# Kernel tuning notes

Measured on AMD Instinct MI355X. Metric: run time of the kernel, lower is better.

Reference implementation:

```python
import jax, jax.numpy as jnp
import numpy as np

N_NODES = 100000
N_EDGES = 1600000


def gcn_conv(x, W, b, src, dst, ew, n):
    """PyG GCNConv: x@W, symmetric deg^-1/2 norm with self-loops, scatter-add at dst, +b."""
    loop = jnp.arange(n, dtype=src.dtype)
    s = jnp.concatenate([src, loop])            # sources incl. self-loops
    d = jnp.concatenate([dst, loop])            # targets incl. self-loops
    w = jnp.concatenate([ew, jnp.ones((n,), ew.dtype)])  # self-loop weight = 1
    deg = jax.ops.segment_sum(w, d, num_segments=n)      # weighted in-degree
    dinv = jnp.where(deg > 0, jax.lax.rsqrt(deg), 0.0)
    norm = dinv[s] * w * dinv[d]                # [E+N]
    h = x @ W                                   # [N, F_out]
    msg = h[s] * norm[:, None]                  # gather + per-edge scale
    out = jax.ops.segment_sum(msg, d, num_segments=n)    # scatter-add
    return out + b


def setup_inputs() -> dict:
    key = jax.random.key(0)
    ks = jax.random.split(key, 8)
    in_dim, hid, lat = 128, 128, 64
    x = jax.random.normal(ks[0], (N_NODES, in_dim), jnp.float32)
    edge_index = jax.random.randint(ks[1], (2, N_EDGES), 0, N_NODES, dtype=jnp.int32)
    weights = jax.random.uniform(ks[2], (N_EDGES,), jnp.float32)
    s_in = 1.0 / np.sqrt(in_dim)
    s_h = 1.0 / np.sqrt(hid)
    return {
        "x": x,
        "edge_index": edge_index,
        "weights": weights,
        "W1": jax.random.normal(ks[3], (in_dim, hid), jnp.float32) * s_in,
        "b1": jnp.zeros((hid,), jnp.float32),
        "W2": jax.random.normal(ks[4], (hid, hid), jnp.float32) * s_h,
        "b2": jnp.zeros((hid,), jnp.float32),
        "W_mu": jax.random.normal(ks[5], (hid, lat), jnp.float32) * s_h,
        "b_mu": jnp.zeros((lat,), jnp.float32),
        "W_lv": jax.random.normal(ks[6], (hid, lat), jnp.float32) * s_h,
        "b_lv": jnp.zeros((lat,), jnp.float32),
    }


def reference(x, edge_index, weights, W1, b1, W2, b2, W_mu, b_mu, W_lv, b_lv):
    n = x.shape[0]
    src, dst = edge_index[0], edge_index[1]
    h = jax.nn.relu(gcn_conv(x, W1, b1, src, dst, weights, n))
    h = gcn_conv(h, W2, b2, src, dst, weights, n)
    g = jnp.mean(h, axis=0, keepdims=True)      # [1, hid] global mean pool
    mu = g @ W_mu + b_mu
    logvar = g @ W_lv + b_lv
    return (mu, logvar)
```

## Files before the change

kernel.cpp:

```cpp
#include <hip/hip_runtime.h>


typedef __bf16 bf16x8 __attribute__((ext_vector_type(8)));
typedef float f32x4 __attribute__((ext_vector_type(4)));
typedef float f32x2 __attribute__((ext_vector_type(2)));
typedef unsigned long long u64;

#define RE   2048
#define BSH  8
#define BCAP 5120
#define NBMX 392

__device__ __forceinline__ float bf2f(unsigned short u){
  return __uint_as_float(((unsigned)u) << 16);
}
__device__ __forceinline__ unsigned short f2bf(float f){
  unsigned u = __float_as_uint(f);
  u += 0x7fffu + ((u >> 16) & 1u);
  return (unsigned short)(u >> 16);
}
__device__ __forceinline__ __bf16 us2bf(unsigned short u){
  __bf16 b; __builtin_memcpy(&b, &u, 2); return b;
}
__device__ __forceinline__ float ldf(const void* p, int i, int isf32){
  return isf32 ? ((const float*)p)[i] : bf2f(((const unsigned short*)p)[i]);
}
__device__ __forceinline__ void fma8f8(float* acc, float n, uint2 h){
  f32x2 p0 = __builtin_amdgcn_cvt_pk_f32_fp8((int)h.x, false);
  f32x2 p1 = __builtin_amdgcn_cvt_pk_f32_fp8((int)h.x, true);
  f32x2 p2 = __builtin_amdgcn_cvt_pk_f32_fp8((int)h.y, false);
  f32x2 p3 = __builtin_amdgcn_cvt_pk_f32_fp8((int)h.y, true);
  acc[0] = fmaf(n, p0[0], acc[0]);
  acc[1] = fmaf(n, p0[1], acc[1]);
  acc[2] = fmaf(n, p1[0], acc[2]);
  acc[3] = fmaf(n, p1[1], acc[3]);
  acc[4] = fmaf(n, p2[0], acc[4]);
  acc[5] = fmaf(n, p2[1], acc[5]);
  acc[6] = fmaf(n, p3[0], acc[6]);
  acc[7] = fmaf(n, p3[1], acc[7]);
}

__device__ __forceinline__ void scanBuckets(int* __restrict__ cnt, int* __restrict__ sm,
    int* __restrict__ hrow, int* __restrict__ rrow, int NB, int tid){
  const int K = (NBMX + 255) / 256;
  int c0 = tid * K;
  int loc = 0;
  #pragma unroll
  for (int i = 0; i < K; ++i){
    int j = c0 + i;
    if (j < NB) loc += cnt[j];
  }
  sm[tid] = loc;
  __syncthreads();
  for (int off = 1; off < 256; off <<= 1){
    int tmp = (tid >= off) ? sm[tid - off] : 0;
    __syncthreads();
    sm[tid] += tmp;
    __syncthreads();
  }
  int running = sm[tid] - loc;
  #pragma unroll
  for (int i = 0; i < K; ++i){
    int j = c0 + i;
    if (j < NB){
      int old = cnt[j];
      hrow[j] = old;
      rrow[j] = running;
      cnt[j] = running;
      running += old;
    }
  }
}

__global__ void k_init(const unsigned* __restrict__ xw, int* __restrict__ flag,
                       const void* __restrict__ W1, unsigned short* __restrict__ W1T,
                       float* __restrict__ v){
  __shared__ int s[256];
  int t = threadIdx.x;
  int cnt = 0;
  for (int k = t; k < 4096; k += 256){
    unsigned lo = xw[k] & 0xFFFFu;
    int e = (int)((lo >> 7) & 0xFFu);
    if ((e >= 100 && e <= 141) || (lo & 0x7FFFu) == 0) cnt++;
  }
  s[t] = cnt;
  __syncthreads();
  for (int off = 128; off > 0; off >>= 1){
    if (t < off) s[t] += s[t + off];
    __syncthreads();
  }
  int isf32 = (s[0] < 2458) ? 1 : 0;
  if (blockIdx.x == 0){
    if (t == 0) *flag = isf32;
    if (t < 128) v[t] = 0.0f;
  }
  int gid = blockIdx.x * 256 + t;
  int k = gid & 127, n = gid >> 7;
  W1T[gid] = isf32 ? f2bf(((const float*)W1)[k * 128 + n])
                   : ((const unsigned short*)W1)[k * 128 + n];
}

__global__ void __launch_bounds__(256) k_binG(const int* __restrict__ src,
    const int* __restrict__ dst, const void* __restrict__ w,
    u64* __restrict__ stagD, u64* __restrict__ stagS,
    int* __restrict__ histD, int* __restrict__ roffD,
    int* __restrict__ histS, int* __restrict__ roffS,
    int E, int NB, int NR,
    const void* __restrict__ xv, const __bf16* __restrict__ wt,
    unsigned char* __restrict__ H, int N, const int* __restrict__ flagp){
  __shared__ int cntD[NBMX];
  __shared__ int cntS[NBMX];
  __shared__ u64 stag[RE];
  __shared__ int sm[256];
  int tid = threadIdx.x;
  if ((int)blockIdx.x >= NR){
    int gb = (int)blockIdx.x - NR;
    int wave = (gb * 256 + tid) >> 6;
    int lane = tid & 63;
    int row16 = wave << 4;
    if (row16 >= N) return;
    int isf32 = *flagp;
    int m = lane & 15, q = lane >> 4;
    bf16x8 a0, a1, a2, a3;
    if (isf32){
      const float* ap = (const float*)xv + (size_t)(row16 + m) * 128 + q * 8;
      #pragma unroll
      for (int j = 0; j < 8; ++j){
        a0[j] = us2bf(f2bf(ap[j +  0]));
        a1[j] = us2bf(f2bf(ap[j + 32]));
        a2[j] = us2bf(f2bf(ap[j + 64]));
        a3[j] = us2bf(f2bf(ap[j + 96]));
      }
    } else {
      const __bf16* ap = (const __bf16*)xv + (size_t)(row16 + m) * 128 + q * 8;
      a0 = *(const bf16x8*)(ap +  0);
      a1 = *(const bf16x8*)(ap + 32);
      a2 = *(const bf16x8*)(ap + 64);
      a3 = *(const bf16x8*)(ap + 96);
    }
    for (int nt = 0; nt < 8; ++nt){
      const __bf16* bp = wt + (size_t)(nt * 16 + m) * 128 + q * 8;
      bf16x8 b0 = *(const bf16x8*)(bp +  0);
      bf16x8 b1 = *(const bf16x8*)(bp + 32);
      bf16x8 b2 = *(const bf16x8*)(bp + 64);
      bf16x8 b3 = *(const bf16x8*)(bp + 96);
      f32x4 acc = {0.f, 0.f, 0.f, 0.f};
      acc = __builtin_amdgcn_mfma_f32_16x16x32_bf16(a0, b0, acc, 0, 0, 0);
      acc = __builtin_amdgcn_mfma_f32_16x16x32_bf16(a1, b1, acc, 0, 0, 0);
      acc = __builtin_amdgcn_mfma_f32_16x16x32_bf16(a2, b2, acc, 0, 0, 0);
      acc = __builtin_amdgcn_mfma_f32_16x16x32_bf16(a3, b3, acc, 0, 0, 0);
      unsigned char* op = H + (size_t)(row16 + q * 4) * 128 + nt * 16 + m;
      op[0]   = (unsigned char)(__builtin_amdgcn_cvt_pk_fp8_f32(acc[0], acc[0], 0, false) & 0xFF);
      op[128] = (unsigned char)(__builtin_amdgcn_cvt_pk_fp8_f32(acc[1], acc[1], 0, false) & 0xFF);
      op[256] = (unsigned char)(__builtin_amdgcn_cvt_pk_fp8_f32(acc[2], acc[2], 0, false) & 0xFF);
      op[384] = (unsigned char)(__builtin_amdgcn_cvt_pk_fp8_f32(acc[3], acc[3], 0, false) & 0xFF);
    }
    return;
  }
  int r = blockIdx.x;
  for (int i = tid; i < NB; i += 256){ cntD[i] = 0; cntS[i] = 0; }
  __syncthreads();
  int isf32 = *flagp;
  int e0 = r * RE;
  int en = E - e0; if (en > RE) en = RE;
  u64 rec[8];
  #pragma unroll
  for (int k = 0; k < 8; ++k){
    int o = k * 256 + tid;
    rec[k] = ~0ull;
    if (o < en){
      int idx = e0 + o;
      int s_ = src[idx], d_ = dst[idx];
      float wf = ldf(w, idx, isf32);
      int wq = (int)(wf * 32768.0f + 0.5f);
      if (wq > 32767) wq = 32767;
      rec[k] = ((u64)(unsigned)d_ << 32) | ((u64)(unsigned)s_ << 15) | (unsigned)wq;
      atomicAdd(&cntD[d_ >> BSH], 1);
      atomicAdd(&cntS[s_ >> BSH], 1);
    }
  }
  __syncthreads();
  scanBuckets(cntD, sm, histD + (size_t)r * NB, roffD + (size_t)r * NB, NB, tid);
  __syncthreads();
  #pragma unroll
  for (int k = 0; k < 8; ++k){
    if (rec[k] != ~0ull){
      int p = atomicAdd(&cntD[(int)(rec[k] >> 32) >> BSH], 1);
      stag[p] = rec[k];
    }
  }
  __syncthreads();
  u64* opD = stagD + (size_t)r * RE;
  for (int i = tid; i < en; i += 256) opD[i] = stag[i];
  __syncthreads();
  scanBuckets(cntS, sm, histS + (size_t)r * NB, roffS + (size_t)r * NB, NB, tid);
  __syncthreads();
  #pragma unroll
  for (int k = 0; k < 8; ++k){
    if (rec[k] != ~0ull){
      int d_ = (int)(rec[k] >> 32);
      int s_ = (int)((rec[k] >> 15) & 0x1FFFFu);
      unsigned wq = (unsigned)(rec[k] & 32767u);
      u64 rs = ((u64)(unsigned)s_ << 32) | ((u64)(unsigned)d_ << 15) | wq;
      int p = atomicAdd(&cntS[s_ >> BSH], 1);
      stag[p] = rs;
    }
  }
  __syncthreads();
  u64* opS = stagS + (size_t)r * RE;
  for (int i = tid; i < en; i += 256) opS[i] = stag[i];
}

__global__ void __launch_bounds__(256) k_transp4(const int* __restrict__ A,
    const int* __restrict__ B, const int* __restrict__ C, const int* __restrict__ D,
    int* __restrict__ AT, int* __restrict__ BT, int* __restrict__ CT,
    int* __restrict__ DT, int NR, int NB){
  __shared__ int ta[32][33];
  __shared__ int tb[32][33];
  __shared__ int tc[32][33];
  __shared__ int td[32][33];
  int bx = (int)blockIdx.x * 32;
  int by = (int)blockIdx.y * 32;
  int tx = threadIdx.x & 31, ty = threadIdx.x >> 5;
  for (int yy = ty; yy < 32; yy += 8){
    int r = by + yy, b = bx + tx;
    int v1 = 0, v2 = 0, v3 = 0, v4 = 0;
    if (r < NR && b < NB){
      size_t o = (size_t)r * NB + b;
      v1 = A[o]; v2 = B[o]; v3 = C[o]; v4 = D[o];
    }
    ta[yy][tx] = v1; tb[yy][tx] = v2; tc[yy][tx] = v3; td[yy][tx] = v4;
  }
  __syncthreads();
  for (int yy = ty; yy < 32; yy += 8){
    int b = bx + yy, r = by + tx;
    if (b < NB && r < NR){
      size_t o = (size_t)b * NR + r;
      AT[o] = ta[tx][yy]; BT[o] = tb[tx][yy];
      CT[o] = tc[tx][yy]; DT[o] = td[tx][yy];
    }
  }
}

__global__ void __launch_bounds__(512) k_pass2a(const u64* __restrict__ staging,
    const int* __restrict__ histT, const int* __restrict__ roffT,
    float* __restrict__ dinv, int* __restrict__ cnt, int* __restrict__ rowptr,
    int* __restrict__ bsum, int NR, int N){
  __shared__ unsigned cd[256];
  __shared__ int sm[512];
  int b = blockIdx.x, tid = threadIdx.x;
  int lo = b << BSH;
  int nn = N - lo; if (nn > 256) nn = 256;
  if (tid < 256) cd[tid] = 0u;
  __syncthreads();
  const int* hrow = histT + (size_t)b * NR;
  const int* rrow = roffT + (size_t)b * NR;
  for (int r = tid; r < NR; r += 512){
    int len = hrow[r];
    if (len == 0) continue;
    const u64* rp = staging + (size_t)r * RE + rrow[r];
    for (int k = 0; k < len; ++k){
      u64 rec = rp[k];
      int dl = (int)(rec >> 32) - lo;
      atomicAdd(&cd[dl], (1u << 20) | (unsigned)((rec & 32767u) >> 2));
    }
  }
  __syncthreads();
  int val = 0;
  if (tid < nn){
    unsigned p = cd[tid];
    dinv[lo + tid] = rsqrtf(1.0f + (float)(p & 0xFFFFFu) * (1.0f / 8192.0f));
    cnt[lo + tid] = (int)(p >> 20);
    val = (int)(p >> 20);
  }
  sm[tid] = val;
  __syncthreads();
  for (int off = 1; off < 512; off <<= 1){
    int tmp = (tid >= off) ? sm[tid - off] : 0;
    __syncthreads();
    sm[tid] += tmp;
    __syncthreads();
  }
  if (tid < nn) rowptr[lo + tid] = sm[tid] - val;
  if (tid == 511) bsum[b] = sm[511];
}

__global__ void k_scanB(const int* __restrict__ bsum, int* __restrict__ boffs, int NB){
  __shared__ int s[512];
  int t = threadIdx.x;
  int val = (t < NB) ? bsum[t] : 0;
  s[t] = val;
  __syncthreads();
  for (int off = 1; off < 512; off <<= 1){
    int tmp = (t >= off) ? s[t - off] : 0;
    __syncthreads();
    s[t] += tmp;
    __syncthreads();
  }
  boffs[t] = s[t] - val;
}

__global__ void k_scanC(int* __restrict__ rowptr, const int* __restrict__ boffs,
                        unsigned* __restrict__ edges, int E, int N){
  if (blockIdx.x == 0 && threadIdx.x >= 240)
    edges[E + threadIdx.x - 240] = 0u;
  int i = blockIdx.x * 256 + threadIdx.x;
  if (i >= N) return;
  rowptr[i] = rowptr[i] + boffs[blockIdx.x];
}

__global__ void __launch_bounds__(512) k_post(const u64* __restrict__ stagD,
    const int* __restrict__ histDT, const int* __restrict__ roffDT,
    const u64* __restrict__ stagS, const int* __restrict__ histST,
    const int* __restrict__ roffST, const float* __restrict__ dinv,
    const int* __restrict__ rowptr, const int* __restrict__ cnt,
    unsigned* __restrict__ edges, float2* __restrict__ dc, int2* __restrict__ rc,
    int NR, int N){
  __shared__ unsigned recs[BCAP];
  __shared__ int cur[256];
  __shared__ int sb[2];
  int b = (int)blockIdx.x >> 1, tid = threadIdx.x;
  int lo = b << BSH;
  int nn = N - lo; if (nn > 256) nn = 256;
  if (blockIdx.x & 1){
    float* SL = (float*)recs;
    if (tid < 256) SL[tid] = 0.0f;
    __syncthreads();
    const int* hrow = histST + (size_t)b * NR;
    const int* rrow = roffST + (size_t)b * NR;
    for (int r = tid; r < NR; r += 512){
      int len = hrow[r];
      if (len == 0) continue;
      const u64* rp = stagS + (size_t)r * RE + rrow[r];
      for (int k = 0; k < len; ++k){
        u64 rec = rp[k];
        int s_ = (int)(rec >> 32);
        int d_ = (int)((rec >> 15) & 0x1FFFFu);
        float wqf = (float)(rec & 32767u) * (1.0f / 32768.0f);
        atomicAdd(&SL[s_ - lo], wqf * dinv[d_]);
      }
    }
    __syncthreads();
    if (tid < nn){
      int i = lo + tid;
      float di = dinv[i];
      dc[i] = make_float2(di * di, di * di + di * SL[tid]);
      rc[i] = make_int2(rowptr[i], cnt[i]);
    }
    return;
  }
  if (tid == 0){
    int base = rowptr[lo];
    sb[0] = base;
    sb[1] = rowptr[lo + nn - 1] + cnt[lo + nn - 1] - base;
  }
  __syncthreads();
  int base = sb[0], tot = sb[1];
  if (tot > BCAP) tot = BCAP;
  if (tid < nn) cur[tid] = rowptr[lo + tid] - base;
  __syncthreads();
  const int* hrow = histDT + (size_t)b * NR;
  const int* rrow = roffDT + (size_t)b * NR;
  for (int r = tid; r < NR; r += 512){
    int len = hrow[r];
    if (len == 0) continue;
    const u64* rp = stagD + (size_t)r * RE + rrow[r];
    for (int k = 0; k < len; ++k){
      u64 rec = rp[k];
      int d_ = (int)(rec >> 32);
      int s_ = (int)((rec >> 15) & 0x1FFFFu);
      int wq = (int)(rec & 32767u);
      float nrm = dinv[s_] * ((float)wq * (1.0f / 32768.0f)) * dinv[d_];
      int nq = (int)(nrm * 32768.0f + 0.5f);
      if (nq > 32767) nq = 32767;
      int p = atomicAdd(&cur[d_ - lo], 1);
      if (p < BCAP) recs[p] = ((unsigned)s_ << 15) | (unsigned)nq;
    }
  }
  __syncthreads();
  unsigned* op = edges + base;
  for (int i = tid; i < tot; i += 512) op[i] = recs[i];
}

__global__ void __launch_bounds__(256) k_agg(const unsigned char* __restrict__ H,
    const int2* __restrict__ rc, const float2* __restrict__ dc,
    const unsigned* __restrict__ edges, const void* __restrict__ b1,
    float* __restrict__ v, int N, int totslots, const int* __restrict__ flagp){
  __shared__ float vsh[128];
  __shared__ float bsh[128];
  int tid = threadIdx.x;
  int isf32 = *flagp;
  if (tid < 128){ vsh[tid] = 0.0f; bsh[tid] = ldf(b1, tid, isf32); }
  __syncthreads();
  int lane = tid & 63;
  int wv = tid >> 6;
  int slot = lane >> 3;
  int q = lane & 7;
  const unsigned char* Hq = H + q * 16;
  float ax[16];
  #pragma unroll
  for (int j = 0; j < 16; ++j) ax[j] = 0.0f;
  int d = ((int)blockIdx.x * 4 + wv) * 8 + slot;
  int2 rcv = make_int2(0, 0); float2 dcv = make_float2(0.f, 0.f);
  uint4 hs = make_uint4(0u, 0u, 0u, 0u);
  if (d < N){
    rcv = rc[d]; dcv = dc[d];
    hs = *(const uint4*)(Hq + (size_t)d * 128);
  }
  while (d < N){
    int dn = d + totslots;
    int2 rcn = make_int2(0, 0); float2 dcn = make_float2(0.f, 0.f);
    uint4 hsn = make_uint4(0u, 0u, 0u, 0u);
    if (dn < N){
      rcn = rc[dn]; dcn = dc[dn];
      hsn = *(const uint4*)(Hq + (size_t)dn * 128);
    }
    float acc[16];
    #pragma unroll
    for (int j = 0; j < 16; ++j) acc[j] = 0.0f;
    fma8f8(acc,     dcv.x, make_uint2(hs.x, hs.y));
    fma8f8(acc + 8, dcv.x, make_uint2(hs.z, hs.w));
    int start = rcv.x, len = rcv.y;
    if (len > 0){
      const unsigned* ep = edges + start;
      unsigned e0 = ep[0], e1 = ep[1], e2 = ep[2], e3 = ep[3];
      uint4 h0 = *(const uint4*)(Hq + (size_t)(e0 >> 15) * 128);
      uint4 h1 = *(const uint4*)(Hq + (size_t)(e1 >> 15) * 128);
      uint4 h2 = *(const uint4*)(Hq + (size_t)(e2 >> 15) * 128);
      #pragma unroll 2
      for (int k = 0; k < len; ++k){
        unsigned en = ep[k + 4];
        uint4 hn = *(const uint4*)(Hq + (size_t)(e3 >> 15) * 128);
        float wn = (float)(e0 & 32767u) * (1.0f / 32768.0f);
        fma8f8(acc,     wn, make_uint2(h0.x, h0.y));
        fma8f8(acc + 8, wn, make_uint2(h0.z, h0.w));
        e0 = e1; e1 = e2; e2 = e3; e3 = en;
        h0 = h1; h1 = h2; h2 = hn;
      }
    }
    #pragma unroll
    for (int j = 0; j < 16; ++j){
      float rj = fmaxf(acc[j] + bsh[q * 16 + j], 0.0f);
      ax[j] = fmaf(dcv.y, rj, ax[j]);
    }
    d = dn; rcv = rcn; dcv = dcn; hs = hsn;
  }
  #pragma unroll
  for (int j = 0; j < 16; ++j){
    ax[j] += __shfl_xor(ax[j], 8);
    ax[j] += __shfl_xor(ax[j], 16);
    ax[j] += __shfl_xor(ax[j], 32);
  }
  if (slot == 0){
    #pragma unroll
    for (int j = 0; j < 16; ++j) atomicAdd(&vsh[q * 16 + j], ax[j]);
  }
  __syncthreads();
  if (tid < 128) atomicAdd(&v[tid], vsh[tid]);
}

__global__ void __launch_bounds__(128) k_head(const float* __restrict__ v,
    const void* __restrict__ W2, const void* __restrict__ b2,
    const void* __restrict__ Wmu, const void* __restrict__ bmu,
    const void* __restrict__ Wlv, const void* __restrict__ blv,
    void* __restrict__ outv, float invN, const int* __restrict__ flagp){
  __shared__ float gsh[128];
  __shared__ float tsh[128];
  int t = threadIdx.x;
  int isf32 = *flagp;
  gsh[t] = v[t] * invN;
  __syncthreads();
  float acc = ldf(b2, t, isf32);
  for (int k = 0; k < 128; ++k) acc = fmaf(gsh[k], ldf(W2, k * 128 + t, isf32), acc);
  tsh[t] = acc;
  __syncthreads();
  int j = t & 63;
  const void* Wp = (t < 64) ? Wmu : Wlv;
  float o = ldf((t < 64) ? bmu : blv, j, isf32);
  for (int k = 0; k < 128; ++k) o = fmaf(tsh[k], ldf(Wp, k * 64 + j, isf32), o);
  if (isf32) ((float*)outv)[t] = o;
  else       ((unsigned short*)outv)[t] = f2bf(o);
}

extern "C" void kernel_launch(void* const* d_in, const int* in_sizes, int n_in,
                              void* d_out, int out_size, void* d_ws, size_t ws_size,
                              hipStream_t stream) {
  const void* x   = d_in[0];
  const int*  ei  = (const int*)d_in[1];
  const void* w   = d_in[2];
  const void* W1  = d_in[3];
  const void* b1  = d_in[4];
  const void* W2  = d_in[5];
  const void* b2  = d_in[6];
  const void* Wmu = d_in[7];
  const void* bmu = d_in[8];
  const void* Wlv = d_in[9];
  const void* blv = d_in[10];

  const int N = in_sizes[0] / 128;
  const int E = in_sizes[2];
  const int* src = ei;
  const int* dst = ei + E;

  char* wsb = (char*)d_ws;
  size_t off = 0;
  auto alloc = [&](size_t bytes) -> void* {
    off = (off + 255) & ~(size_t)255;
    void* p = wsb + off;
    off += bytes;
    return p;
  };
  const int NR  = (E + RE - 1) / RE;
  const int NB  = (N + 255) >> BSH;
  int*   flag     = (int*)  alloc(16);
  float* dinv     = (float*)alloc((size_t)N * 4);
  int*   cnt      = (int*)  alloc((size_t)N * 4);
  int*   rowptr   = (int*)  alloc((size_t)(N + 1) * 4);
  float2* dc      = (float2*)alloc((size_t)N * 8);
  int2*   rc      = (int2*) alloc((size_t)N * 8);
  int*   bsum     = (int*)  alloc(512 * 4);
  int*   boffs    = (int*)  alloc(512 * 4);
  float* v        = (float*)alloc(128 * 4);
  unsigned short* W1T = (unsigned short*)alloc(128 * 128 * 2);
  u64*   stagD    = (u64*)  alloc((size_t)NR * RE * 8);
  u64*   stagS    = (u64*)  alloc((size_t)NR * RE * 8);
  int*   histD    = (int*)  alloc((size_t)NR * NB * 4);
  int*   roffD    = (int*)  alloc((size_t)NR * NB * 4);
  int*   histS    = (int*)  alloc((size_t)NR * NB * 4);
  int*   roffS    = (int*)  alloc((size_t)NR * NB * 4);
  int*   histDT   = (int*)  alloc((size_t)NB * NR * 4);
  int*   roffDT   = (int*)  alloc((size_t)NB * NR * 4);
  int*   histST   = (int*)  alloc((size_t)NB * NR * 4);
  int*   roffST   = (int*)  alloc((size_t)NB * NR * 4);
  unsigned* edges = (unsigned*)alloc((size_t)E * 4 + 64);
  unsigned char* H = (unsigned char*)alloc((size_t)N * 128);
  (void)ws_size; (void)n_in; (void)out_size;

  const int nb_n = (N + 255) / 256;
  const int nwaves = (N + 15) / 16;
  const int nb_g = (nwaves + 3) / 4;

  k_init<<<64, 256, 0, stream>>>((const unsigned*)x, flag, W1, W1T, v);
  k_binG<<<NR + nb_g, 256, 0, stream>>>(src, dst, w, stagD, stagS,
                                        histD, roffD, histS, roffS, E, NB, NR,
                                        x, (const __bf16*)W1T, H, N, flag);
  dim3 tg((NB + 31) / 32, (NR + 31) / 32);
  k_transp4<<<tg, 256, 0, stream>>>(histD, roffD, histS, roffS,
                                    histDT, roffDT, histST, roffST, NR, NB);
  k_pass2a<<<NB, 512, 0, stream>>>(stagD, histDT, roffDT, dinv, cnt, rowptr,
                                   bsum, NR, N);
  k_scanB<<<1, 512, 0, stream>>>(bsum, boffs, NB);
  k_scanC<<<nb_n, 256, 0, stream>>>(rowptr, boffs, edges, E, N);
  k_post<<<2 * NB, 512, 0, stream>>>(stagD, histDT, roffDT, stagS, histST,
                                     roffST, dinv, rowptr, cnt, edges, dc, rc,
                                     NR, N);
  const int nb_agg = 1024;
  k_agg<<<nb_agg, 256, 0, stream>>>(H, rc, dc, edges, b1, v, N, nb_agg * 32, flag);
  k_head<<<1, 128, 0, stream>>>(v, W2, b2, Wmu, bmu, Wlv, blv,
                                d_out, 1.0f / (float)N, flag);
}
```

Before: 315.1 us.

## Fold CSR build into per-bucket padded layout and prescale H by dinv

```diff
diff --git a/kernel.cpp b/kernel.cpp
--- a/kernel.cpp
+++ b/kernel.cpp
@@ -100,22 +100,185 @@
                    : ((const unsigned short*)W1)[k * 128 + n];
 }
 
-__global__ void __launch_bounds__(256) k_binG(const int* __restrict__ src,
+__global__ void __launch_bounds__(256) k_bin(const int* __restrict__ src,
     const int* __restrict__ dst, const void* __restrict__ w,
     u64* __restrict__ stagD, u64* __restrict__ stagS,
     int* __restrict__ histD, int* __restrict__ roffD,
     int* __restrict__ histS, int* __restrict__ roffS,
-    int E, int NB, int NR,
-    const void* __restrict__ xv, const __bf16* __restrict__ wt,
-    unsigned char* __restrict__ H, int N, const int* __restrict__ flagp){
+    int E, int NB, const int* __restrict__ flagp){
   __shared__ int cntD[NBMX];
   __shared__ int cntS[NBMX];
   __shared__ u64 stag[RE];
   __shared__ int sm[256];
   int tid = threadIdx.x;
-  if ((int)blockIdx.x >= NR){
-    int gb = (int)blockIdx.x - NR;
-    int wave = (gb * 256 + tid) >> 6;
+  int r = blockIdx.x;
+  for (int i = tid; i < NB; i += 256){ cntD[i] = 0; cntS[i] = 0; }
+  __syncthreads();
+  int isf32 = *flagp;
+  int e0 = r * RE;
+  int en = E - e0; if (en > RE) en = RE;
+  u64 rec[8];
+  #pragma unroll
+  for (int k = 0; k < 8; ++k){
+    int o = k * 256 + tid;
+    rec[k] = ~0ull;
+    if (o < en){
+      int idx = e0 + o;
+      int s_ = src[idx], d_ = dst[idx];
+      float wf = ldf(w, idx, isf32);
+      int wq = (int)(wf * 32768.0f + 0.5f);
+      if (wq > 32767) wq = 32767;
+      rec[k] = ((u64)(unsigned)d_ << 32) | ((u64)(unsigned)s_ << 15) | (unsigned)wq;
+      atomicAdd(&cntD[d_ >> BSH], 1);
+      atomicAdd(&cntS[s_ >> BSH], 1);
+    }
+  }
+  __syncthreads();
+  scanBuckets(cntD, sm, histD + (size_t)r * NB, roffD + (size_t)r * NB, NB, tid);
+  __syncthreads();
+  #pragma unroll
+  for (int k = 0; k < 8; ++k){
+    if (rec[k] != ~0ull){
+      int p = atomicAdd(&cntD[(int)(rec[k] >> 32) >> BSH], 1);
+      stag[p] = rec[k];
+    }
+  }
+  __syncthreads();
+  u64* opD = stagD + (size_t)r * RE;
+  for (int i = tid; i < en; i += 256) opD[i] = stag[i];
+  __syncthreads();
+  scanBuckets(cntS, sm, histS + (size_t)r * NB, roffS + (size_t)r * NB, NB, tid);
+  __syncthreads();
+  #pragma unroll
+  for (int k = 0; k < 8; ++k){
+    if (rec[k] != ~0ull){
+      int d_ = (int)(rec[k] >> 32);
+      int s_ = (int)((rec[k] >> 15) & 0x1FFFFu);
+      unsigned wq = (unsigned)(rec[k] & 32767u);
+      u64 rs = ((u64)(unsigned)s_ << 32) | ((u64)(unsigned)d_ << 15) | wq;
+      int p = atomicAdd(&cntS[s_ >> BSH], 1);
+      stag[p] = rs;
+    }
+  }
+  __syncthreads();
+  u64* opS = stagS + (size_t)r * RE;
+  for (int i = tid; i < en; i += 256) opS[i] = stag[i];
+}
+
+__global__ void __launch_bounds__(256) k_transp4(const int* __restrict__ A,
+    const int* __restrict__ B, const int* __restrict__ C, const int* __restrict__ D,
+    int* __restrict__ AT, int* __restrict__ BT, int* __restrict__ CT,
+    int* __restrict__ DT, int NR, int NB){
+  __shared__ int ta[32][33];
+  __shared__ int tb[32][33];
+  __shared__ int tc[32][33];
+  __shared__ int td[32][33];
+  int bx = (int)blockIdx.x * 32;
+  int by = (int)blockIdx.y * 32;
+  int tx = threadIdx.x & 31, ty = threadIdx.x >> 5;
+  for (int yy = ty; yy < 32; yy += 8){
+    int r = by + yy, b = bx + tx;
+    int v1 = 0, v2 = 0, v3 = 0, v4 = 0;
+    if (r < NR && b < NB){
+      size_t o = (size_t)r * NB + b;
+      v1 = A[o]; v2 = B[o]; v3 = C[o]; v4 = D[o];
+    }
+    ta[yy][tx] = v1; tb[yy][tx] = v2; tc[yy][tx] = v3; td[yy][tx] = v4;
+  }
+  __syncthreads();
+  for (int yy = ty; yy < 32; yy += 8){
+    int b = bx + yy, r = by + tx;
+    if (b < NB && r < NR){
+      size_t o = (size_t)b * NR + r;
+      AT[o] = ta[tx][yy]; BT[o] = tb[tx][yy];
+      CT[o] = tc[tx][yy]; DT[o] = td[tx][yy];
+    }
+  }
+}
+
+__global__ void __launch_bounds__(512) k_fold(const u64* __restrict__ stagD,
+    const int* __restrict__ histT, const int* __restrict__ roffT,
+    float* __restrict__ dinv, int2* __restrict__ rc,
+    unsigned* __restrict__ edges, int NR, int N){
+  __shared__ unsigned cd[256];
+  __shared__ float dinvL[256];
+  __shared__ int cur[256];
+  __shared__ int sm[256];
+  __shared__ unsigned recs[BCAP];
+  int b = blockIdx.x, tid = threadIdx.x;
+  int lo = b << BSH;
+  int nn = N - lo; if (nn > 256) nn = 256;
+  if (tid < 256) cd[tid] = 0u;
+  __syncthreads();
+  const int* hrow = histT + (size_t)b * NR;
+  const int* rrow = roffT + (size_t)b * NR;
+  for (int r = tid; r < NR; r += 512){
+    int len = hrow[r];
+    if (len == 0) continue;
+    const u64* rp = stagD + (size_t)r * RE + rrow[r];
+    for (int k = 0; k < len; ++k){
+      u64 rec = rp[k];
+      int dl = (int)(rec >> 32) - lo;
+      atomicAdd(&cd[dl], (1u << 20) | (unsigned)((rec & 32767u) >> 2));
+    }
+  }
+  __syncthreads();
+  int c = 0;
+  if (tid < 256){
+    unsigned p = cd[tid];
+    float di = rsqrtf(1.0f + (float)(p & 0xFFFFFu) * (1.0f / 8192.0f));
+    dinvL[tid] = di;
+    c = (int)(p >> 20);
+    if (tid < nn) dinv[lo + tid] = di;
+    sm[tid] = c;
+  }
+  __syncthreads();
+  for (int off = 1; off < 256; off <<= 1){
+    int tmp = (tid < 256 && tid >= off) ? sm[tid - off] : 0;
+    __syncthreads();
+    if (tid < 256) sm[tid] += tmp;
+    __syncthreads();
+  }
+  if (tid < 256){
+    int pre = sm[tid] - c;
+    cur[tid] = pre;
+    if (tid < nn) rc[lo + tid] = make_int2(b * BCAP + pre, c);
+  }
+  __syncthreads();
+  int tot = sm[255];
+  for (int r = tid; r < NR; r += 512){
+    int len = hrow[r];
+    if (len == 0) continue;
+    const u64* rp = stagD + (size_t)r * RE + rrow[r];
+    for (int k = 0; k < len; ++k){
+      u64 rec = rp[k];
+      int dl = (int)(rec >> 32) - lo;
+      int s_ = (int)((rec >> 15) & 0x1FFFFu);
+      int wq = (int)(rec & 32767u);
+      int nq = (int)((float)wq * dinvL[dl] + 0.5f);
+      if (nq > 32767) nq = 32767;
+      int p = atomicAdd(&cur[dl], 1);
+      if (p < BCAP) recs[p] = ((unsigned)s_ << 15) | (unsigned)nq;
+    }
+  }
+  __syncthreads();
+  if (tid < 16 && tot + tid < BCAP) recs[tot + tid] = 0u;
+  __syncthreads();
+  int lim = tot + 16; if (lim > BCAP) lim = BCAP;
+  unsigned* op = edges + (size_t)b * BCAP;
+  for (int i = tid; i < lim; i += 512) op[i] = recs[i];
+}
+
+__global__ void __launch_bounds__(256) k_postG(const void* __restrict__ xv,
+    const __bf16* __restrict__ wt, unsigned char* __restrict__ H,
+    const u64* __restrict__ stagS, const int* __restrict__ histST,
+    const int* __restrict__ roffST, const float* __restrict__ dinv,
+    float2* __restrict__ dc, int nbg, int NR, int N,
+    const int* __restrict__ flagp){
+  __shared__ float SL[256];
+  int tid = threadIdx.x;
+  if ((int)blockIdx.x < nbg){
+    int wave = ((int)blockIdx.x * 256 + tid) >> 6;
     int lane = tid & 63;
     int row16 = wave << 4;
     if (row16 >= N) return;
@@ -138,6 +301,7 @@
       a2 = *(const bf16x8*)(ap + 64);
       a3 = *(const bf16x8*)(ap + 96);
     }
+    float4 dv = *(const float4*)(dinv + row16 + q * 4);
     for (int nt = 0; nt < 8; ++nt){
       const __bf16* bp = wt + (size_t)(nt * 16 + m) * 128 + q * 8;
       bf16x8 b0 = *(const bf16x8*)(bp +  0);
@@ -150,236 +314,40 @@
       acc = __builtin_amdgcn_mfma_f32_16x16x32_bf16(a2, b2, acc, 0, 0, 0);
       acc = __builtin_amdgcn_mfma_f32_16x16x32_bf16(a3, b3, acc, 0, 0, 0);
       unsigned char* op = H + (size_t)(row16 + q * 4) * 128 + nt * 16 + m;
-      op[0]   = (unsigned char)(__builtin_amdgcn_cvt_pk_fp8_f32(acc[0], acc[0], 0, false) & 0xFF);
-      op[128] = (unsigned char)(__builtin_amdgcn_cvt_pk_fp8_f32(acc[1], acc[1], 0, false) & 0xFF);
-      op[256] = (unsigned char)(__builtin_amdgcn_cvt_pk_fp8_f32(acc[2], acc[2], 0, false) & 0xFF);
-      op[384] = (unsigned char)(__builtin_amdgcn_cvt_pk_fp8_f32(acc[3], acc[3], 0, false) & 0xFF);
+      float v0 = acc[0] * dv.x, v1 = acc[1] * dv.y;
+      float v2 = acc[2] * dv.z, v3 = acc[3] * dv.w;
+      op[0]   = (unsigned char)(__builtin_amdgcn_cvt_pk_fp8_f32(v0, v0, 0, false) & 0xFF);
+      op[128] = (unsigned char)(__builtin_amdgcn_cvt_pk_fp8_f32(v1, v1, 0, false) & 0xFF);
+      op[256] = (unsigned char)(__builtin_amdgcn_cvt_pk_fp8_f32(v2, v2, 0, false) & 0xFF);
+      op[384] = (unsigned char)(__builtin_amdgcn_cvt_pk_fp8_f32(v3, v3, 0, false) & 0xFF);
     }
     return;
   }
-  int r = blockIdx.x;
-  for (int i = tid; i < NB; i += 256){ cntD[i] = 0; cntS[i] = 0; }
-  __syncthreads();
-  int isf32 = *flagp;
-  int e0 = r * RE;
-  int en = E - e0; if (en > RE) en = RE;
-  u64 rec[8];
-  #pragma unroll
-  for (int k = 0; k < 8; ++k){
-    int o = k * 256 + tid;
-    rec[k] = ~0ull;
-    if (o < en){
-      int idx = e0 + o;
-      int s_ = src[idx], d_ = dst[idx];
-      float wf = ldf(w, idx, isf32);
-      int wq = (int)(wf * 32768.0f + 0.5f);
-      if (wq > 32767) wq = 32767;
-      rec[k] = ((u64)(unsigned)d_ << 32) | ((u64)(unsigned)s_ << 15) | (unsigned)wq;
-      atomicAdd(&cntD[d_ >> BSH], 1);
-      atomicAdd(&cntS[s_ >> BSH], 1);
-    }
-  }
-  __syncthreads();
-  scanBuckets(cntD, sm, histD + (size_t)r * NB, roffD + (size_t)r * NB, NB, tid);
-  __syncthreads();
-  #pragma unroll
-  for (int k = 0; k < 8; ++k){
-    if (rec[k] != ~0ull){
-      int p = atomicAdd(&cntD[(int)(rec[k] >> 32) >> BSH], 1);
-      stag[p] = rec[k];
-    }
-  }
-  __syncthreads();
-  u64* opD = stagD + (size_t)r * RE;
-  for (int i = tid; i < en; i += 256) opD[i] = stag[i];
-  __syncthreads();
-  scanBuckets(cntS, sm, histS + (size_t)r * NB, roffS + (size_t)r * NB, NB, tid);
-  __syncthreads();
-  #pragma unroll
-  for (int k = 0; k < 8; ++k){
-    if (rec[k] != ~0ull){
-      int d_ = (int)(rec[k] >> 32);
-      int s_ = (int)((rec[k] >> 15) & 0x1FFFFu);
-      unsigned wq = (unsigned)(rec[k] & 32767u);
-      u64 rs = ((u64)(unsigned)s_ << 32) | ((u64)(unsigned)d_ << 15) | wq;
-      int p = atomicAdd(&cntS[s_ >> BSH], 1);
-      stag[p] = rs;
-    }
-  }
-  __syncthreads();
-  u64* opS = stagS + (size_t)r * RE;
-  for (int i = tid; i < en; i += 256) opS[i] = stag[i];
-}
-
-__global__ void __launch_bounds__(256) k_transp4(const int* __restrict__ A,
-    const int* __restrict__ B, const int* __restrict__ C, const int* __restrict__ D,
-    int* __restrict__ AT, int* __restrict__ BT, int* __restrict__ CT,
-    int* __restrict__ DT, int NR, int NB){
-  __shared__ int ta[32][33];
-  __shared__ int tb[32][33];
-  __shared__ int tc[32][33];
-  __shared__ int td[32][33];
-  int bx = (int)blockIdx.x * 32;
-  int by = (int)blockIdx.y * 32;
-  int tx = threadIdx.x & 31, ty = threadIdx.x >> 5;
-  for (int yy = ty; yy < 32; yy += 8){
-    int r = by + yy, b = bx + tx;
-    int v1 = 0, v2 = 0, v3 = 0, v4 = 0;
-    if (r < NR && b < NB){
-      size_t o = (size_t)r * NB + b;
-      v1 = A[o]; v2 = B[o]; v3 = C[o]; v4 = D[o];
-    }
-    ta[yy][tx] = v1; tb[yy][tx] = v2; tc[yy][tx] = v3; td[yy][tx] = v4;
-  }
-  __syncthreads();
-  for (int yy = ty; yy < 32; yy += 8){
-    int b = bx + yy, r = by + tx;
-    if (b < NB && r < NR){
-      size_t o = (size_t)b * NR + r;
-      AT[o] = ta[tx][yy]; BT[o] = tb[tx][yy];
-      CT[o] = tc[tx][yy]; DT[o] = td[tx][yy];
-    }
-  }
-}
-
-__global__ void __launch_bounds__(512) k_pass2a(const u64* __restrict__ staging,
-    const int* __restrict__ histT, const int* __restrict__ roffT,
-    float* __restrict__ dinv, int* __restrict__ cnt, int* __restrict__ rowptr,
-    int* __restrict__ bsum, int NR, int N){
-  __shared__ unsigned cd[256];
-  __shared__ int sm[512];
-  int b = blockIdx.x, tid = threadIdx.x;
+  int b = (int)blockIdx.x - nbg;
   int lo = b << BSH;
   int nn = N - lo; if (nn > 256) nn = 256;
-  if (tid < 256) cd[tid] = 0u;
-  __syncthreads();
-  const int* hrow = histT + (size_t)b * NR;
-  const int* rrow = roffT + (size_t)b * NR;
-  for (int r = tid; r < NR; r += 512){
+  if (tid < 256) SL[tid] = 0.0f;
+  __syncthreads();
+  const int* hrow = histST + (size_t)b * NR;
+  const int* rrow = roffST + (size_t)b * NR;
+  for (int r = tid; r < NR; r += 256){
     int len = hrow[r];
     if (len == 0) continue;
-    const u64* rp = staging + (size_t)r * RE + rrow[r];
+    const u64* rp = stagS + (size_t)r * RE + rrow[r];
     for (int k = 0; k < len; ++k){
       u64 rec = rp[k];
-      int dl = (int)(rec >> 32) - lo;
-      atomicAdd(&cd[dl], (1u << 20) | (unsigned)((rec & 32767u) >> 2));
-    }
-  }
-  __syncthreads();
-  int val = 0;
+      int s_ = (int)(rec >> 32);
+      int d_ = (int)((rec >> 15) & 0x1FFFFu);
+      float wqf = (float)(rec & 32767u) * (1.0f / 32768.0f);
+      atomicAdd(&SL[s_ - lo], wqf * dinv[d_]);
+    }
+  }
+  __syncthreads();
   if (tid < nn){
-    unsigned p = cd[tid];
-    dinv[lo + tid] = rsqrtf(1.0f + (float)(p & 0xFFFFFu) * (1.0f / 8192.0f));
-    cnt[lo + tid] = (int)(p >> 20);
-    val = (int)(p >> 20);
-  }
-  sm[tid] = val;
-  __syncthreads();
-  for (int off = 1; off < 512; off <<= 1){
-    int tmp = (tid >= off) ? sm[tid - off] : 0;
-    __syncthreads();
-    sm[tid] += tmp;
-    __syncthreads();
-  }
-  if (tid < nn) rowptr[lo + tid] = sm[tid] - val;
-  if (tid == 511) bsum[b] = sm[511];
-}
-
-__global__ void k_scanB(const int* __restrict__ bsum, int* __restrict__ boffs, int NB){
-  __shared__ int s[512];
-  int t = threadIdx.x;
-  int val = (t < NB) ? bsum[t] : 0;
-  s[t] = val;
-  __syncthreads();
-  for (int off = 1; off < 512; off <<= 1){
-    int tmp = (t >= off) ? s[t - off] : 0;
-    __syncthreads();
-    s[t] += tmp;
-    __syncthreads();
-  }
-  boffs[t] = s[t] - val;
-}
-
-__global__ void k_scanC(int* __restrict__ rowptr, const int* __restrict__ boffs,
-                        unsigned* __restrict__ edges, int E, int N){
-  if (blockIdx.x == 0 && threadIdx.x >= 240)
-    edges[E + threadIdx.x - 240] = 0u;
-  int i = blockIdx.x * 256 + threadIdx.x;
-  if (i >= N) return;
-  rowptr[i] = rowptr[i] + boffs[blockIdx.x];
-}
-
-__global__ void __launch_bounds__(512) k_post(const u64* __restrict__ stagD,
-    const int* __restrict__ histDT, const int* __restrict__ roffDT,
-    const u64* __restrict__ stagS, const int* __restrict__ histST,
-    const int* __restrict__ roffST, const float* __restrict__ dinv,
-    const int* __restrict__ rowptr, const int* __restrict__ cnt,
-    unsigned* __restrict__ edges, float2* __restrict__ dc, int2* __restrict__ rc,
-    int NR, int N){
-  __shared__ unsigned recs[BCAP];
-  __shared__ int cur[256];
-  __shared__ int sb[2];
-  int b = (int)blockIdx.x >> 1, tid = threadIdx.x;
-  int lo = b << BSH;
-  int nn = N - lo; if (nn > 256) nn = 256;
-  if (blockIdx.x & 1){
-    float* SL = (float*)recs;
-    if (tid < 256) SL[tid] = 0.0f;
-    __syncthreads();
-    const int* hrow = histST + (size_t)b * NR;
-    const int* rrow = roffST + (size_t)b * NR;
-    for (int r = tid; r < NR; r += 512){
-      int len = hrow[r];
-      if (len == 0) continue;
-      const u64* rp = stagS + (size_t)r * RE + rrow[r];
-      for (int k = 0; k < len; ++k){
-        u64 rec = rp[k];
-        int s_ = (int)(rec >> 32);
-        int d_ = (int)((rec >> 15) & 0x1FFFFu);
-        float wqf = (float)(rec & 32767u) * (1.0f / 32768.0f);
-        atomicAdd(&SL[s_ - lo], wqf * dinv[d_]);
-      }
-    }
-    __syncthreads();
-    if (tid < nn){
-      int i = lo + tid;
-      float di = dinv[i];
-      dc[i] = make_float2(di * di, di * di + di * SL[tid]);
-      rc[i] = make_int2(rowptr[i], cnt[i]);
-    }
-    return;
-  }
-  if (tid == 0){
-    int base = rowptr[lo];
-    sb[0] = base;
-    sb[1] = rowptr[lo + nn - 1] + cnt[lo + nn - 1] - base;
-  }
-  __syncthreads();
-  int base = sb[0], tot = sb[1];
-  if (tot > BCAP) tot = BCAP;
-  if (tid < nn) cur[tid] = rowptr[lo + tid] - base;
-  __syncthreads();
-  const int* hrow = histDT + (size_t)b * NR;
-  const int* rrow = roffDT + (size_t)b * NR;
-  for (int r = tid; r < NR; r += 512){
-    int len = hrow[r];
-    if (len == 0) continue;
-    const u64* rp = stagD + (size_t)r * RE + rrow[r];
-    for (int k = 0; k < len; ++k){
-      u64 rec = rp[k];
-      int d_ = (int)(rec >> 32);
-      int s_ = (int)((rec >> 15) & 0x1FFFFu);
-      int wq = (int)(rec & 32767u);
-      float nrm = dinv[s_] * ((float)wq * (1.0f / 32768.0f)) * dinv[d_];
-      int nq = (int)(nrm * 32768.0f + 0.5f);
-      if (nq > 32767) nq = 32767;
-      int p = atomicAdd(&cur[d_ - lo], 1);
-      if (p < BCAP) recs[p] = ((unsigned)s_ << 15) | (unsigned)nq;
-    }
-  }
-  __syncthreads();
-  unsigned* op = edges + base;
-  for (int i = tid; i < tot; i += 512) op[i] = recs[i];
+    int i = lo + tid;
+    float di = dinv[i];
+    dc[i] = make_float2(di, di * di + di * SL[tid]);
+  }
 }
 
 __global__ void __launch_bounds__(256) k_agg(const unsigned char* __restrict__ H,
@@ -513,13 +481,9 @@
   const int NR  = (E + RE - 1) / RE;
   const int NB  = (N + 255) >> BSH;
   int*   flag     = (int*)  alloc(16);
-  float* dinv     = (float*)alloc((size_t)N * 4);
-  int*   cnt      = (int*)  alloc((size_t)N * 4);
-  int*   rowptr   = (int*)  alloc((size_t)(N + 1) * 4);
+  float* dinv     = (float*)alloc((size_t)N * 4 + 16);
   float2* dc      = (float2*)alloc((size_t)N * 8);
   int2*   rc      = (int2*) alloc((size_t)N * 8);
-  int*   bsum     = (int*)  alloc(512 * 4);
-  int*   boffs    = (int*)  alloc(512 * 4);
   float* v        = (float*)alloc(128 * 4);
   unsigned short* W1T = (unsigned short*)alloc(128 * 128 * 2);
   u64*   stagD    = (u64*)  alloc((size_t)NR * RE * 8);
@@ -532,28 +496,23 @@
   int*   roffDT   = (int*)  alloc((size_t)NB * NR * 4);
   int*   histST   = (int*)  alloc((size_t)NB * NR * 4);
   int*   roffST   = (int*)  alloc((size_t)NB * NR * 4);
-  unsigned* edges = (unsigned*)alloc((size_t)E * 4 + 64);
+  unsigned* edges = (unsigned*)alloc((size_t)NB * BCAP * 4 + 64);
   unsigned char* H = (unsigned char*)alloc((size_t)N * 128);
   (void)ws_size; (void)n_in; (void)out_size;
 
-  const int nb_n = (N + 255) / 256;
   const int nwaves = (N + 15) / 16;
   const int nb_g = (nwaves + 3) / 4;
 
   k_init<<<64, 256, 0, stream>>>((const unsigned*)x, flag, W1, W1T, v);
-  k_binG<<<NR + nb_g, 256, 0, stream>>>(src, dst, w, stagD, stagS,
-                                        histD, roffD, histS, roffS, E, NB, NR,
-                                        x, (const __bf16*)W1T, H, N, flag);
+  k_bin<<<NR, 256, 0, stream>>>(src, dst, w, stagD, stagS,
+                                histD, roffD, histS, roffS, E, NB, flag);
   dim3 tg((NB + 31) / 32, (NR + 31) / 32);
   k_transp4<<<tg, 256, 0, stream>>>(histD, roffD, histS, roffS,
                                     histDT, roffDT, histST, roffST, NR, NB);
-  k_pass2a<<<NB, 512, 0, stream>>>(stagD, histDT, roffDT, dinv, cnt, rowptr,
-                                   bsum, NR, N);
-  k_scanB<<<1, 512, 0, stream>>>(bsum, boffs, NB);
-  k_scanC<<<nb_n, 256, 0, stream>>>(rowptr, boffs, edges, E, N);
-  k_post<<<2 * NB, 512, 0, stream>>>(stagD, histDT, roffDT, stagS, histST,
-                                     roffST, dinv, rowptr, cnt, edges, dc, rc,
-                                     NR, N);
+  k_fold<<<NB, 512, 0, stream>>>(stagD, histDT, roffDT, dinv, rc, edges, NR, N);
+  k_postG<<<nb_g + NB, 256, 0, stream>>>(x, (const __bf16*)W1T, H,
+                                         stagS, histST, roffST, dinv, dc,
+                                         nb_g, NR, N, flag);
   const int nb_agg = 1024;
   k_agg<<<nb_agg, 256, 0, stream>>>(H, rc, dc, edges, b1, v, N, nb_agg * 32, flag);
   k_head<<<1, 128, 0, stream>>>(v, W2, b2, Wmu, bmu, Wlv, blv,
```

After: 300.8 us. 4.6% less time.
